# Performance work log

Hardware: AMD Instinct MI355X
Metric: run time of the kernel (lower is better)

Reference implementation:

```python
import jax, jax.numpy as jnp
import numpy as np

D = 32          # embedding_size
B = 16384       # batch_size
P = 16          # neighbor_sample_size (paths per item per hop)
NE = 100000     # n_entity
NU = 100000     # n_user
NR = 32         # n_relation
N_ITER = 2


def setup_inputs() -> dict:
    key = jax.random.key(0)
    ks = jax.random.split(key, 20)
    s = 0.1
    nrm = lambda k, sh: jax.random.normal(k, sh, dtype=jnp.float32) * s
    inp = {
        "user_table": nrm(ks[0], (NU, D)),
        "ent_table": nrm(ks[1], (NE, D)),
        "rel_table": nrm(ks[2], (NR, D)),
        # PyTorch LSTM params, gate order (i, f, g, o)
        "w_ih0": nrm(ks[3], (4 * D, 2 * D)),
        "w_hh0": nrm(ks[4], (4 * D, D)),
        "b_ih0": nrm(ks[5], (4 * D,)),
        "b_hh0": nrm(ks[6], (4 * D,)),
        "w_ih1": nrm(ks[7], (4 * D, 2 * D)),
        "w_hh1": nrm(ks[8], (4 * D, D)),
        "b_ih1": nrm(ks[9], (4 * D,)),
        "b_hh1": nrm(ks[10], (4 * D,)),
        "agg_w": nrm(ks[11], (D, D)),
        "agg_b": nrm(ks[12], (D,)),
        "users": jax.random.randint(ks[13], (B,), 0, NU),
        "items": jax.random.randint(ks[14], (B,), 0, NE),
        "ratings": jax.random.randint(ks[15], (B,), 0, 2),
        # hop h path table: [n_entity, P, 2*(h+1)+1]; values < 32 valid for both tables
        "lp0": jax.random.randint(ks[16], (NE, P, 3), 0, 32),
        "lp1": jax.random.randint(ks[17], (NE, P, 5), 0, 32),
    }
    return inp


def _lstm_last(seq, w_ih, w_hh, b_ih, b_hh):
    # seq: [N, T, 2D] -> final hidden state [N, D], PyTorch gate order i,f,g,o
    N = seq.shape[0]
    H = w_hh.shape[1]
    bias = b_ih + b_hh

    def step(carry, x):
        h, c = carry
        g = x @ w_ih.T + h @ w_hh.T + bias
        i, f, gg, o = jnp.split(g, 4, axis=-1)
        c = jax.nn.sigmoid(f) * c + jax.nn.sigmoid(i) * jnp.tanh(gg)
        h = jax.nn.sigmoid(o) * jnp.tanh(c)
        return (h, c), None

    h0 = jnp.zeros((N, H), seq.dtype)
    (h, _), _ = jax.lax.scan(step, (h0, h0), jnp.swapaxes(seq, 0, 1))
    return h


def _forward(user_table, ent_table, rel_table, lstm_params, agg_w, agg_b,
             users, items, ratings, lps):
    u = user_table[users]                # [B, D]
    items_emb = ent_table[items]         # [B, D]
    for hop in range(N_ITER):
        lp = lps[hop]
        w_ih, w_hh, b_ih, b_hh = lstm_params[hop]
        il = lp[items]                   # [B, P, 2*(hop+1)+1]
        seed_e = ent_table[il[:, :, 0]]  # [B, P, D]
        u_b = jnp.broadcast_to(u[:, None, :], seed_e.shape)
        first = jnp.concatenate([u_b, seed_e], -1)[:, :, None, :]   # [B,P,1,2D]
        rel_e = rel_table[il[:, :, 1::2]]                            # [B,P,hop+1,D]
        tail_e = ent_table[il[:, :, 2::2]]                           # [B,P,hop+1,D]
        rest = jnp.concatenate([rel_e, tail_e], -1)                  # [B,P,hop+1,2D]
        seq = jnp.concatenate([first, rest], 2).reshape(B * P, hop + 2, 2 * D)
        h = _lstm_last(seq, w_ih, w_hh, b_ih, b_hh)                  # [B*P, D]
        final = h.reshape(B, P, D).sum(axis=1)                       # hidden_out sum
        items_emb = (items_emb + final) @ agg_w.T + agg_b            # 'sum' aggregator
    scores = jnp.sum(u * items_emb, axis=-1)                         # [B]
    r = ratings.astype(scores.dtype)
    # stable BCE on sigmoid(scores)
    loss = -jnp.mean(r * jax.nn.log_sigmoid(scores) + (1.0 - r) * jax.nn.log_sigmoid(-scores))
    return loss, jax.nn.sigmoid(scores)


def reference(user_table, ent_table, rel_table,
              w_ih0, w_hh0, b_ih0, b_hh0,
              w_ih1, w_hh1, b_ih1, b_hh1,
              agg_w, agg_b,
              users, items, ratings, lp0, lp1):
    lstm_params = [(w_ih0, w_hh0, b_ih0, b_hh0), (w_ih1, w_hh1, b_ih1, b_hh1)]
    loss, scores_normalized = _forward(user_table, ent_table, rel_table,
                                       lstm_params, agg_w, agg_b,
                                       users, items, ratings, (lp0, lp1))
    return (loss, scores_normalized, items)
```

## Files before the change

kernel.cpp:

```cpp
#include <hip/hip_runtime.h>
#include <math.h>

#define D  32
#define BN 16384
#define PP 16

typedef __bf16 bf16x8 __attribute__((ext_vector_type(8)));
typedef __bf16 bf16x4 __attribute__((ext_vector_type(4)));
typedef float  floatx4 __attribute__((ext_vector_type(4)));

#define K1 1.44269504088896341f
#define K2 2.88539008177792681f

#define WU_OFF     0
#define WHH_OFF    10240
#define T0T_OFF    20480
#define TRT_OFF    30720
#define IMG_BYTES  40960
#define H_OFF      40960
#define LDS_BYTES  (IMG_BYTES + 8 * 1280)

__device__ __forceinline__ float sigf(float x) {
    float e = __builtin_amdgcn_exp2f(-x * K1);
    return __builtin_amdgcn_rcpf(1.0f + e);
}
__device__ __forceinline__ float logsigf(float x) {
    float ax = fabsf(x);
    float l = log1pf(__expf(-ax));
    return (x >= 0.0f) ? -l : x - l;
}
__device__ __forceinline__ bf16x8 loadu8(const float* __restrict__ p) {
    float4 a = ((const float4*)p)[0], b = ((const float4*)p)[1];
    bf16x8 r = { (__bf16)a.x, (__bf16)a.y, (__bf16)a.z, (__bf16)a.w,
                 (__bf16)b.x, (__bf16)b.y, (__bf16)b.z, (__bf16)b.w };
    return r;
}

__device__ __forceinline__ bf16x8 onehot8(int sel, int q) {
    union { unsigned w[4]; bf16x8 v; } u;
    const unsigned val = 0x3F80u << ((sel & 1) * 16);
    const int grp = sel >> 1;
    #pragma unroll
    for (int wd = 0; wd < 4; ++wd)
        u.w[wd] = (grp == q * 4 + wd) ? val : 0u;
    return u.v;
}

__global__ __launch_bounds__(256)
void prep_tables(const float* __restrict__ ent, const float* __restrict__ rel,
                 const float* __restrict__ wih0, const float* __restrict__ whh0,
                 const float* __restrict__ bih0, const float* __restrict__ bhh0,
                 const float* __restrict__ wih1, const float* __restrict__ whh1,
                 const float* __restrict__ bih1, const float* __restrict__ bhh1,
                 const int* __restrict__ items,
                 const int* __restrict__ lp0, const int* __restrict__ lp1,
                 char* __restrict__ imgs, int* __restrict__ pidx,
                 float* __restrict__ out)
{
    const int id = blockIdx.x * 256 + threadIdx.x;
    if (id < 16384) {
        const int hop  = id >> 13;
        const int rest = id & 8191;
        const int mat  = rest >> 12;
        const int e    = rest & 4095;
        const int gate = e >> 5, d = e & 31;
        float v = mat ? (hop ? whh1 : whh0)[(size_t)gate * 32 + d]
                      : (hop ? wih1 : wih0)[(size_t)gate * 64 + d];
        __bf16* dst = (__bf16*)(imgs + hop * IMG_BYTES + (mat ? WHH_OFF : WU_OFF));
        dst[gate * 40 + d] = (__bf16)v;
    } else if (id < 24576) {
        const int idb = id - 16384;
        const int hop = idb >> 12;
        const int g   = (idb >> 5) & 127;
        const int k   = idb & 31;
        const float* wih = hop ? wih1 : wih0;
        const float4* w4 = (const float4*)(wih + (size_t)g * 64 + 32);
        const float4* e4 = (const float4*)(ent + (size_t)k * 32);
        float a = hop ? bih1[g] + bhh1[g] : bih0[g] + bhh0[g];
        #pragma unroll
        for (int i = 0; i < 8; ++i) {
            float4 w = w4[i], x = e4[i];
            a = fmaf(w.x, x.x, a); a = fmaf(w.y, x.y, a);
            a = fmaf(w.z, x.z, a); a = fmaf(w.w, x.w, a);
        }
        ((__bf16*)(imgs + hop * IMG_BYTES + T0T_OFF))[g * 40 + k] = (__bf16)a;
    } else if (id < 32768) {
        const int idb = id - 24576;
        const int hop = idb >> 12;
        const int g   = (idb >> 5) & 127;
        const int j   = idb & 31;
        const float* wih = hop ? wih1 : wih0;
        const float4* w4 = (const float4*)(wih + (size_t)g * 64);
        const float4* r4 = (const float4*)(rel + (size_t)j * 32);
        float a = 0.0f;
        #pragma unroll
        for (int i = 0; i < 8; ++i) {
            float4 w = w4[i], x = r4[i];
            a = fmaf(w.x, x.x, a); a = fmaf(w.y, x.y, a);
            a = fmaf(w.z, x.z, a); a = fmaf(w.w, x.w, a);
        }
        ((__bf16*)(imgs + hop * IMG_BYTES + TRT_OFF))[g * 40 + j] = (__bf16)a;
    } else if (id < 32768 + 524288) {
        const int c   = id - 32768;
        const int hop = c >> 18;
        const int rem = c & 262143;
        const int fb  = rem >> 4;
        const int p   = rem & 15;
        const int item = items[fb];
        int w;
        if (hop == 0) {
            const int* il = lp0 + ((size_t)item * PP + p) * 3;
            w = il[0] | (il[1] << 5) | (il[2] << 10);
        } else {
            const int* il = lp1 + ((size_t)item * PP + p) * 5;
            w = il[0] | (il[1] << 5) | (il[2] << 10) | (il[3] << 15)
                      | (il[4] << 20);
        }
        pidx[(size_t)(hop * BN + fb) * PP + p] = w;
    } else if (id == 32768 + 524288) {
        out[0] = 0.0f;
    }
}

template<bool FIRST, bool LAST>
__device__ __forceinline__ void nonlin(
    floatx4* __restrict__ acc, float* __restrict__ cst,
    float* __restrict__ hlo, float* __restrict__ hhi,
    char* __restrict__ Hw, int q, int bnl)
{
    #pragma unroll
    for (int hf = 0; hf < 2; ++hf) {
        float* hout = hf ? hhi : hlo;
        #pragma unroll
        for (int r = 0; r < 4; ++r) {
            float gi = acc[0 + hf][r], gf = acc[2 + hf][r],
                  gg = acc[4 + hf][r], go = acc[6 + hf][r];
            float Ai = 1.0f + __builtin_amdgcn_exp2f(-gi * K1);
            float Af = 1.0f + __builtin_amdgcn_exp2f(-gf * K1);
            float G2 = __builtin_amdgcn_exp2f(gg * K2);
            float Gp = G2 + 1.0f, Gm = G2 - 1.0f;
            float cold = FIRST ? 0.0f : cst[hf * 4 + r];
            float num = cold * Ai * Gp + Gm * Af;
            float c = num * __builtin_amdgcn_rcpf(Af * Ai * Gp);
            cst[hf * 4 + r] = c;
            float Ao = 1.0f + __builtin_amdgcn_exp2f(-go * K1);
            float C2 = __builtin_amdgcn_exp2f(c * K2);
            hout[r] = (C2 - 1.0f) * __builtin_amdgcn_rcpf(Ao * (C2 + 1.0f));
        }
    }
    if (!LAST) {
        bf16x4 plo = { (__bf16)hlo[0], (__bf16)hlo[1], (__bf16)hlo[2], (__bf16)hlo[3] };
        bf16x4 phi = { (__bf16)hhi[0], (__bf16)hhi[1], (__bf16)hhi[2], (__bf16)hhi[3] };
        *(bf16x4*)(Hw + bnl * 80 + 8 * q)      = plo;
        *(bf16x4*)(Hw + bnl * 80 + 32 + 8 * q) = phi;
    }
}

__global__ __launch_bounds__(256, 3)
void hop_mfma(const float* __restrict__ user_table,
              const int*   __restrict__ users,
              const int*   __restrict__ pidx,
              const char*  __restrict__ imgs,
              float* __restrict__ F0,
              float* __restrict__ F1)
{
    __shared__ __align__(16) char lds[LDS_BYTES];

    const bool second = blockIdx.x & 1;
    const int  idx    = blockIdx.x >> 1;
    const int tid  = threadIdx.x;
    const int lane = tid & 63;
    const int wave = tid >> 6;
    const int q    = lane >> 4;
    const int bnl  = lane & 15;

    const int fbA = idx * 8 + wave;
    const int fbB = fbA + 4;
    const int ixA = pidx[(size_t)((second ? BN : 0) + fbA) * PP + bnl];
    const int ixB = pidx[(size_t)((second ? BN : 0) + fbB) * PP + bnl];
    bf16x8 buA = loadu8(user_table + (size_t)users[fbA] * D + q * 8);
    bf16x8 buB = loadu8(user_table + (size_t)users[fbB] * D + q * 8);

    {
        const float4* g4 = (const float4*)(imgs + (second ? IMG_BYTES : 0));
        float4* l4 = (float4*)lds;
        #pragma unroll
        for (int i = 0; i < 10; ++i) l4[i * 256 + tid] = g4[i * 256 + tid];
    }
    const char* Wu  = lds + WU_OFF;
    const char* Whh = lds + WHH_OFF;
    const char* T0t = lds + T0T_OFF;
    const char* TRt = lds + TRT_OFF;
    char* HwA = lds + H_OFF + (wave * 2 + 0) * 1280;
    char* HwB = lds + H_OFF + (wave * 2 + 1) * 1280;

    __syncthreads();

    float cstA[8], cstB[8], hloA[4], hhiA[4], hloB[4], hhiB[4];
    const floatx4 zf4 = { 0.0f, 0.0f, 0.0f, 0.0f };

    {
        bf16x8 ohA = onehot8(ixA & 31, q);
        bf16x8 ohB = onehot8(ixB & 31, q);
        floatx4 accA[8], accB[8];
        #pragma unroll
        for (int mt = 0; mt < 8; ++mt) {
            const int ro = (16 * mt + bnl) * 80 + q * 16;
            bf16x8 t0f = *(const bf16x8*)(T0t + ro);
            bf16x8 wuf = *(const bf16x8*)(Wu  + ro);
            accA[mt] = __builtin_amdgcn_mfma_f32_16x16x32_bf16(t0f, ohA, zf4, 0, 0, 0);
            accB[mt] = __builtin_amdgcn_mfma_f32_16x16x32_bf16(t0f, ohB, zf4, 0, 0, 0);
            accA[mt] = __builtin_amdgcn_mfma_f32_16x16x32_bf16(wuf, buA, accA[mt], 0, 0, 0);
            accB[mt] = __builtin_amdgcn_mfma_f32_16x16x32_bf16(wuf, buB, accB[mt], 0, 0, 0);
        }
        nonlin<true, false>(accA, cstA, hloA, hhiA, HwA, q, bnl);
        nonlin<true, false>(accB, cstB, hloB, hhiB, HwB, q, bnl);
    }

    {
        bf16x8 ohjA = onehot8((ixA >> 5) & 31, q);
        bf16x8 ohkA = onehot8((ixA >> 10) & 31, q);
        bf16x8 ohjB = onehot8((ixB >> 5) & 31, q);
        bf16x8 ohkB = onehot8((ixB >> 10) & 31, q);
        bf16x8 bhA = *(const bf16x8*)(HwA + bnl * 80 + q * 16);
        bf16x8 bhB = *(const bf16x8*)(HwB + bnl * 80 + q * 16);
        floatx4 accA[8], accB[8];
        #pragma unroll
        for (int mt = 0; mt < 8; ++mt) {
            const int ro = (16 * mt + bnl) * 80 + q * 16;
            bf16x8 trf = *(const bf16x8*)(TRt + ro);
            bf16x8 t0f = *(const bf16x8*)(T0t + ro);
            bf16x8 whf = *(const bf16x8*)(Whh + ro);
            accA[mt] = __builtin_amdgcn_mfma_f32_16x16x32_bf16(trf, ohjA, zf4, 0, 0, 0);
            accB[mt] = __builtin_amdgcn_mfma_f32_16x16x32_bf16(trf, ohjB, zf4, 0, 0, 0);
            accA[mt] = __builtin_amdgcn_mfma_f32_16x16x32_bf16(t0f, ohkA, accA[mt], 0, 0, 0);
            accB[mt] = __builtin_amdgcn_mfma_f32_16x16x32_bf16(t0f, ohkB, accB[mt], 0, 0, 0);
            accA[mt] = __builtin_amdgcn_mfma_f32_16x16x32_bf16(whf, bhA, accA[mt], 0, 0, 0);
            accB[mt] = __builtin_amdgcn_mfma_f32_16x16x32_bf16(whf, bhB, accB[mt], 0, 0, 0);
        }
        if (second) {
            nonlin<false, false>(accA, cstA, hloA, hhiA, HwA, q, bnl);
            nonlin<false, false>(accB, cstB, hloB, hhiB, HwB, q, bnl);
        } else {
            nonlin<false, true>(accA, cstA, hloA, hhiA, HwA, q, bnl);
            nonlin<false, true>(accB, cstB, hloB, hhiB, HwB, q, bnl);
        }
    }

    if (second) {
        bf16x8 ohjA = onehot8((ixA >> 15) & 31, q);
        bf16x8 ohkA = onehot8((ixA >> 20) & 31, q);
        bf16x8 ohjB = onehot8((ixB >> 15) & 31, q);
        bf16x8 ohkB = onehot8((ixB >> 20) & 31, q);
        bf16x8 bhA = *(const bf16x8*)(HwA + bnl * 80 + q * 16);
        bf16x8 bhB = *(const bf16x8*)(HwB + bnl * 80 + q * 16);
        floatx4 accA[8], accB[8];
        #pragma unroll
        for (int mt = 0; mt < 8; ++mt) {
            const int ro = (16 * mt + bnl) * 80 + q * 16;
            bf16x8 trf = *(const bf16x8*)(TRt + ro);
            bf16x8 t0f = *(const bf16x8*)(T0t + ro);
            bf16x8 whf = *(const bf16x8*)(Whh + ro);
            accA[mt] = __builtin_amdgcn_mfma_f32_16x16x32_bf16(trf, ohjA, zf4, 0, 0, 0);
            accB[mt] = __builtin_amdgcn_mfma_f32_16x16x32_bf16(trf, ohjB, zf4, 0, 0, 0);
            accA[mt] = __builtin_amdgcn_mfma_f32_16x16x32_bf16(t0f, ohkA, accA[mt], 0, 0, 0);
            accB[mt] = __builtin_amdgcn_mfma_f32_16x16x32_bf16(t0f, ohkB, accB[mt], 0, 0, 0);
            accA[mt] = __builtin_amdgcn_mfma_f32_16x16x32_bf16(whf, bhA, accA[mt], 0, 0, 0);
            accB[mt] = __builtin_amdgcn_mfma_f32_16x16x32_bf16(whf, bhB, accB[mt], 0, 0, 0);
        }
        nonlin<false, true>(accA, cstA, hloA, hhiA, HwA, q, bnl);
        nonlin<false, true>(accB, cstB, hloB, hhiB, HwB, q, bnl);
    }

    #pragma unroll
    for (int r = 0; r < 4; ++r) {
        #pragma unroll
        for (int m = 1; m < 16; m <<= 1) {
            hloA[r] += __shfl_xor(hloA[r], m);
            hhiA[r] += __shfl_xor(hhiA[r], m);
            hloB[r] += __shfl_xor(hloB[r], m);
            hhiB[r] += __shfl_xor(hhiB[r], m);
        }
    }
    if (bnl == 0) {
        float* Fout = (second ? F1 : F0);
        float4 vloA = { hloA[0], hloA[1], hloA[2], hloA[3] };
        float4 vhiA = { hhiA[0], hhiA[1], hhiA[2], hhiA[3] };
        float4 vloB = { hloB[0], hloB[1], hloB[2], hloB[3] };
        float4 vhiB = { hhiB[0], hhiB[1], hhiB[2], hhiB[3] };
        *(float4*)(Fout + (size_t)fbA * D + 4 * q)      = vloA;
        *(float4*)(Fout + (size_t)fbA * D + 16 + 4 * q) = vhiA;
        *(float4*)(Fout + (size_t)fbB * D + 4 * q)      = vloB;
        *(float4*)(Fout + (size_t)fbB * D + 16 + 4 * q) = vhiB;
    }
}

__global__ __launch_bounds__(256)
void chain_score(const float* __restrict__ user_table,
                 const float* __restrict__ ent_table,
                 const float* __restrict__ agg_w,
                 const float* __restrict__ agg_b,
                 const int*   __restrict__ users,
                 const int*   __restrict__ items,
                 const int*   __restrict__ ratings,
                 const float* __restrict__ F0,
                 const float* __restrict__ F1,
                 float* __restrict__ out)
{
    __shared__ float s[8][33];
    __shared__ float red[8];
    const int tid = threadIdx.x;
    const int bb  = tid >> 5;
    const int j   = tid & 31;
    const int b   = blockIdx.x * 8 + bb;
    const int it  = items[b];

    s[bb][j] = ent_table[(size_t)it * D + j] + F0[(size_t)b * D + j];
    __syncthreads();
    const float* __restrict__ w = agg_w + (size_t)j * D;
    float e0 = agg_b[j];
    #pragma unroll
    for (int k = 0; k < D; ++k) e0 = fmaf(s[bb][k], w[k], e0);
    __syncthreads();
    s[bb][j] = e0 + F1[(size_t)b * D + j];
    __syncthreads();
    float e1 = agg_b[j];
    #pragma unroll
    for (int k = 0; k < D; ++k) e1 = fmaf(s[bb][k], w[k], e1);

    float prod = user_table[(size_t)users[b] * D + j] * e1;
    #pragma unroll
    for (int m = 1; m < 32; m <<= 1) prod += __shfl_xor(prod, m);
    if (j == 0) {
        out[1 + b]      = sigf(prod);
        out[1 + BN + b] = (float)it;
        float r = (float)ratings[b];
        red[bb] = r * logsigf(prod) + (1.0f - r) * logsigf(-prod);
    }
    __syncthreads();
    if (tid == 0) {
        float t = 0.0f;
        #pragma unroll
        for (int qq = 0; qq < 8; ++qq) t += red[qq];
        atomicAdd(out, -t / (float)BN);
    }
}

extern "C" void kernel_launch(void* const* d_in, const int* in_sizes, int n_in,
                              void* d_out, int out_size, void* d_ws, size_t ws_size,
                              hipStream_t stream)
{
    const float* user_table = (const float*)d_in[0];
    const float* ent_table  = (const float*)d_in[1];
    const float* rel_table  = (const float*)d_in[2];
    const float* w_ih0 = (const float*)d_in[3];
    const float* w_hh0 = (const float*)d_in[4];
    const float* b_ih0 = (const float*)d_in[5];
    const float* b_hh0 = (const float*)d_in[6];
    const float* w_ih1 = (const float*)d_in[7];
    const float* w_hh1 = (const float*)d_in[8];
    const float* b_ih1 = (const float*)d_in[9];
    const float* b_hh1 = (const float*)d_in[10];
    const float* agg_w = (const float*)d_in[11];
    const float* agg_b = (const float*)d_in[12];
    const int* users   = (const int*)d_in[13];
    const int* items   = (const int*)d_in[14];
    const int* ratings = (const int*)d_in[15];
    const int* lp0     = (const int*)d_in[16];
    const int* lp1     = (const int*)d_in[17];
    float* out = (float*)d_out;

    float* ws   = (float*)d_ws;
    float* F0   = ws;
    float* F1   = F0 + (size_t)BN * D;
    char*  imgs = (char*)(F1 + (size_t)BN * D);
    int*   pidx = (int*)(imgs + 2 * IMG_BYTES);

    prep_tables<<<2177, 256, 0, stream>>>(ent_table, rel_table,
        w_ih0, w_hh0, b_ih0, b_hh0, w_ih1, w_hh1, b_ih1, b_hh1,
        items, lp0, lp1, imgs, pidx, out);
    hop_mfma<<<4096, 256, 0, stream>>>(
        user_table, users, pidx, imgs, F0, F1);
    chain_score<<<BN / 8, 256, 0, stream>>>(
        user_table, ent_table, agg_w, agg_b, users, items, ratings,
        F0, F1, out);
}
```

Before: 240.4 us.

## Precompute user-gate projections in prep kernel and replace loss atomics with reduction

```diff
diff --git a/kernel.cpp b/kernel.cpp
--- a/kernel.cpp
+++ b/kernel.cpp
@@ -12,12 +12,11 @@
 #define K1 1.44269504088896341f
 #define K2 2.88539008177792681f
 
-#define WU_OFF     0
-#define WHH_OFF    10240
-#define T0T_OFF    20480
-#define TRT_OFF    30720
-#define IMG_BYTES  40960
-#define H_OFF      40960
+#define WHH_OFF    0
+#define T0T_OFF    10240
+#define TRT_OFF    20480
+#define IMG_BYTES  30720
+#define H_OFF      30720
 #define LDS_BYTES  (IMG_BYTES + 8 * 1280)
 
 __device__ __forceinline__ float sigf(float x) {
@@ -29,10 +28,8 @@
     float l = log1pf(__expf(-ax));
     return (x >= 0.0f) ? -l : x - l;
 }
-__device__ __forceinline__ bf16x8 loadu8(const float* __restrict__ p) {
-    float4 a = ((const float4*)p)[0], b = ((const float4*)p)[1];
-    bf16x8 r = { (__bf16)a.x, (__bf16)a.y, (__bf16)a.z, (__bf16)a.w,
-                 (__bf16)b.x, (__bf16)b.y, (__bf16)b.z, (__bf16)b.w };
+__device__ __forceinline__ floatx4 cvt4(bf16x4 v) {
+    floatx4 r = { (float)v[0], (float)v[1], (float)v[2], (float)v[3] };
     return r;
 }
 
@@ -47,29 +44,26 @@
 }
 
 __global__ __launch_bounds__(256)
-void prep_tables(const float* __restrict__ ent, const float* __restrict__ rel,
+void prep_tables(const float* __restrict__ user_table,
+                 const float* __restrict__ ent, const float* __restrict__ rel,
                  const float* __restrict__ wih0, const float* __restrict__ whh0,
                  const float* __restrict__ bih0, const float* __restrict__ bhh0,
                  const float* __restrict__ wih1, const float* __restrict__ whh1,
                  const float* __restrict__ bih1, const float* __restrict__ bhh1,
-                 const int* __restrict__ items,
+                 const int* __restrict__ users, const int* __restrict__ items,
                  const int* __restrict__ lp0, const int* __restrict__ lp1,
-                 char* __restrict__ imgs, int* __restrict__ pidx,
-                 float* __restrict__ out)
+                 char* __restrict__ imgs, __bf16* __restrict__ GU,
+                 int* __restrict__ pidx)
 {
     const int id = blockIdx.x * 256 + threadIdx.x;
-    if (id < 16384) {
-        const int hop  = id >> 13;
-        const int rest = id & 8191;
-        const int mat  = rest >> 12;
-        const int e    = rest & 4095;
+    if (id < 8192) {
+        const int hop  = id >> 12;
+        const int e    = id & 4095;
         const int gate = e >> 5, d = e & 31;
-        float v = mat ? (hop ? whh1 : whh0)[(size_t)gate * 32 + d]
-                      : (hop ? wih1 : wih0)[(size_t)gate * 64 + d];
-        __bf16* dst = (__bf16*)(imgs + hop * IMG_BYTES + (mat ? WHH_OFF : WU_OFF));
-        dst[gate * 40 + d] = (__bf16)v;
-    } else if (id < 24576) {
-        const int idb = id - 16384;
+        float v = (hop ? whh1 : whh0)[(size_t)gate * 32 + d];
+        ((__bf16*)(imgs + hop * IMG_BYTES + WHH_OFF))[gate * 40 + d] = (__bf16)v;
+    } else if (id < 16384) {
+        const int idb = id - 8192;
         const int hop = idb >> 12;
         const int g   = (idb >> 5) & 127;
         const int k   = idb & 31;
@@ -84,8 +78,8 @@
             a = fmaf(w.z, x.z, a); a = fmaf(w.w, x.w, a);
         }
         ((__bf16*)(imgs + hop * IMG_BYTES + T0T_OFF))[g * 40 + k] = (__bf16)a;
-    } else if (id < 32768) {
-        const int idb = id - 24576;
+    } else if (id < 24576) {
+        const int idb = id - 16384;
         const int hop = idb >> 12;
         const int g   = (idb >> 5) & 127;
         const int j   = idb & 31;
@@ -100,8 +94,33 @@
             a = fmaf(w.z, x.z, a); a = fmaf(w.w, x.w, a);
         }
         ((__bf16*)(imgs + hop * IMG_BYTES + TRT_OFF))[g * 40 + j] = (__bf16)a;
-    } else if (id < 32768 + 524288) {
-        const int c   = id - 32768;
+    } else if (id < 1073152) {
+        const int c   = id - 24576;
+        const int hop = c >> 19;
+        const int gq  = (c >> 14) & 31;
+        const int fb  = c & 16383;
+        const float* wih = hop ? wih1 : wih0;
+        const float4* u4 = (const float4*)(user_table + (size_t)users[fb] * 32);
+        float4 uu[8];
+        #pragma unroll
+        for (int i = 0; i < 8; ++i) uu[i] = u4[i];
+        __bf16 r[4];
+        #pragma unroll
+        for (int t = 0; t < 4; ++t) {
+            const float4* w4 = (const float4*)(wih + (size_t)(gq * 4 + t) * 64);
+            float a = 0.0f;
+            #pragma unroll
+            for (int i = 0; i < 8; ++i) {
+                float4 w = w4[i];
+                a = fmaf(w.x, uu[i].x, a); a = fmaf(w.y, uu[i].y, a);
+                a = fmaf(w.z, uu[i].z, a); a = fmaf(w.w, uu[i].w, a);
+            }
+            r[t] = (__bf16)a;
+        }
+        bf16x4 v = { r[0], r[1], r[2], r[3] };
+        *(bf16x4*)(GU + ((size_t)(hop * BN + fb) * 128 + gq * 4)) = v;
+    } else if (id < 1597440) {
+        const int c   = id - 1073152;
         const int hop = c >> 18;
         const int rem = c & 262143;
         const int fb  = rem >> 4;
@@ -117,8 +136,6 @@
                       | (il[4] << 20);
         }
         pidx[(size_t)(hop * BN + fb) * PP + p] = w;
-    } else if (id == 32768 + 524288) {
-        out[0] = 0.0f;
     }
 }
 
@@ -156,11 +173,10 @@
     }
 }
 
-__global__ __launch_bounds__(256, 3)
-void hop_mfma(const float* __restrict__ user_table,
-              const int*   __restrict__ users,
-              const int*   __restrict__ pidx,
+__global__ __launch_bounds__(256, 4)
+void hop_mfma(const int*   __restrict__ pidx,
               const char*  __restrict__ imgs,
+              const __bf16* __restrict__ GU,
               float* __restrict__ F0,
               float* __restrict__ F1)
 {
@@ -176,18 +192,25 @@
 
     const int fbA = idx * 8 + wave;
     const int fbB = fbA + 4;
-    const int ixA = pidx[(size_t)((second ? BN : 0) + fbA) * PP + bnl];
-    const int ixB = pidx[(size_t)((second ? BN : 0) + fbB) * PP + bnl];
-    bf16x8 buA = loadu8(user_table + (size_t)users[fbA] * D + q * 8);
-    bf16x8 buB = loadu8(user_table + (size_t)users[fbB] * D + q * 8);
+    const int hbase = second ? BN : 0;
+    const int ixA = pidx[(size_t)(hbase + fbA) * PP + bnl];
+    const int ixB = pidx[(size_t)(hbase + fbB) * PP + bnl];
+    bf16x4 guhA[8], guhB[8];
+    #pragma unroll
+    for (int mt = 0; mt < 8; ++mt) {
+        guhA[mt] = *(const bf16x4*)(GU + ((size_t)(hbase + fbA) * 128 + mt * 16 + q * 4));
+        guhB[mt] = *(const bf16x4*)(GU + ((size_t)(hbase + fbB) * 128 + mt * 16 + q * 4));
+    }
 
     {
         const float4* g4 = (const float4*)(imgs + (second ? IMG_BYTES : 0));
         float4* l4 = (float4*)lds;
         #pragma unroll
-        for (int i = 0; i < 10; ++i) l4[i * 256 + tid] = g4[i * 256 + tid];
-    }
-    const char* Wu  = lds + WU_OFF;
+        for (int i = 0; i < 8; ++i) {
+            int k = i * 256 + tid;
+            if (k < IMG_BYTES / 16) l4[k] = g4[k];
+        }
+    }
     const char* Whh = lds + WHH_OFF;
     const char* T0t = lds + T0T_OFF;
     const char* TRt = lds + TRT_OFF;
@@ -207,11 +230,8 @@
         for (int mt = 0; mt < 8; ++mt) {
             const int ro = (16 * mt + bnl) * 80 + q * 16;
             bf16x8 t0f = *(const bf16x8*)(T0t + ro);
-            bf16x8 wuf = *(const bf16x8*)(Wu  + ro);
-            accA[mt] = __builtin_amdgcn_mfma_f32_16x16x32_bf16(t0f, ohA, zf4, 0, 0, 0);
-            accB[mt] = __builtin_amdgcn_mfma_f32_16x16x32_bf16(t0f, ohB, zf4, 0, 0, 0);
-            accA[mt] = __builtin_amdgcn_mfma_f32_16x16x32_bf16(wuf, buA, accA[mt], 0, 0, 0);
-            accB[mt] = __builtin_amdgcn_mfma_f32_16x16x32_bf16(wuf, buB, accB[mt], 0, 0, 0);
+            accA[mt] = __builtin_amdgcn_mfma_f32_16x16x32_bf16(t0f, ohA, cvt4(guhA[mt]), 0, 0, 0);
+            accB[mt] = __builtin_amdgcn_mfma_f32_16x16x32_bf16(t0f, ohB, cvt4(guhB[mt]), 0, 0, 0);
         }
         nonlin<true, false>(accA, cstA, hloA, hhiA, HwA, q, bnl);
         nonlin<true, false>(accB, cstB, hloB, hhiB, HwB, q, bnl);
@@ -305,7 +325,8 @@
                  const int*   __restrict__ ratings,
                  const float* __restrict__ F0,
                  const float* __restrict__ F1,
-                 float* __restrict__ out)
+                 float* __restrict__ out,
+                 float* __restrict__ partials)
 {
     __shared__ float s[8][33];
     __shared__ float red[8];
@@ -342,8 +363,23 @@
         float t = 0.0f;
         #pragma unroll
         for (int qq = 0; qq < 8; ++qq) t += red[qq];
-        atomicAdd(out, -t / (float)BN);
-    }
+        partials[blockIdx.x] = t;
+    }
+}
+
+__global__ __launch_bounds__(256)
+void loss_kernel(const float* __restrict__ partials, float* __restrict__ out)
+{
+    __shared__ float red[4];
+    const int t = threadIdx.x;
+    float v = 0.0f;
+    #pragma unroll
+    for (int qq = 0; qq < 8; ++qq) v += partials[qq * 256 + t];
+    #pragma unroll
+    for (int m = 1; m < 64; m <<= 1) v += __shfl_xor(v, m);
+    if ((t & 63) == 0) red[t >> 6] = v;
+    __syncthreads();
+    if (t == 0) out[0] = -(red[0] + red[1] + red[2] + red[3]) / (float)BN;
 }
 
 extern "C" void kernel_launch(void* const* d_in, const int* in_sizes, int n_in,
@@ -370,18 +406,20 @@
     const int* lp1     = (const int*)d_in[17];
     float* out = (float*)d_out;
 
-    float* ws   = (float*)d_ws;
-    float* F0   = ws;
-    float* F1   = F0 + (size_t)BN * D;
-    char*  imgs = (char*)(F1 + (size_t)BN * D);
-    int*   pidx = (int*)(imgs + 2 * IMG_BYTES);
-
-    prep_tables<<<2177, 256, 0, stream>>>(ent_table, rel_table,
+    float* ws       = (float*)d_ws;
+    float* F0       = ws;
+    float* F1       = F0 + (size_t)BN * D;
+    float* partials = F1 + (size_t)BN * D;
+    char*  imgs     = (char*)(partials + 2048);
+    int*   pidx     = (int*)(imgs + 2 * IMG_BYTES);
+    __bf16* GU      = (__bf16*)(pidx + 2 * (size_t)BN * PP);
+
+    prep_tables<<<6240, 256, 0, stream>>>(user_table, ent_table, rel_table,
         w_ih0, w_hh0, b_ih0, b_hh0, w_ih1, w_hh1, b_ih1, b_hh1,
-        items, lp0, lp1, imgs, pidx, out);
-    hop_mfma<<<4096, 256, 0, stream>>>(
-        user_table, users, pidx, imgs, F0, F1);
+        users, items, lp0, lp1, imgs, GU, pidx);
+    hop_mfma<<<4096, 256, 0, stream>>>(pidx, imgs, GU, F0, F1);
     chain_score<<<BN / 8, 256, 0, stream>>>(
         user_table, ent_table, agg_w, agg_b, users, items, ratings,
-        F0, F1, out);
-}
+        F0, F1, out, partials);
+    loss_kernel<<<1, 256, 0, stream>>>(partials, out);
+}
```

After: 261.9 us. 9.0% more time.
